# Kernel optimization log

Hardware: AMD Instinct MI355X
Metric: run time of the kernel (lower is better)

The kernel has to match this reference:

```python
import jax, jax.numpy as jnp
import numpy as np

EMBED_DIM = 512
BLOCK = 511
N_HEAD = 8
N_GLOBAL = 4
N_LOCAL = 2
N_MIX = 2
RECEP = 4
T = 2 * BLOCK + 2  # [task, clip, BLOCK upper, BLOCK lower]
HD = EMBED_DIM // N_HEAD
NEG = -1e9


def _build_masks():
    bs = BLOCK
    temporal = np.concatenate([np.zeros(2), np.arange(bs) * 2 + 1, np.arange(bs) * 2 + 2])
    seq = temporal[None, :] <= temporal[:, None]  # causal over interleaved temporal order
    tq = np.concatenate([np.arange(bs) * 2 + 1 - 2 * RECEP + 1] * 2)
    tk = np.concatenate([np.arange(bs) * 2 + 1] * 2)
    de = tk[None, :] < tq[:, None]  # keys too far in the past for the sliding window
    local = seq.copy()
    local[2:, 2:] = local[2:, 2:] & ~de
    return jnp.asarray(local), jnp.asarray(seq)


LOCAL_MASK, GLOBAL_MASK = _build_masks()  # (T, T) bool, True = visible


def _linear_params(key, fan_in, fan_out):
    k1, k2 = jax.random.split(key)
    s = 1.0 / np.sqrt(fan_in)
    W = jax.random.uniform(k1, (fan_out, fan_in), minval=-s, maxval=s, dtype=jnp.float32)
    b = jax.random.uniform(k2, (fan_out,), minval=-s, maxval=s, dtype=jnp.float32)
    return W, b


def setup_inputs() -> dict:
    key = jax.random.key(0)
    ks = jax.random.split(key, 10)
    B = 4
    x = jax.random.normal(ks[0], (B, T, EMBED_DIM), dtype=jnp.float32)
    cond_mask = jnp.ones((B, T), dtype=jnp.float32)
    Wq, bq = _linear_params(ks[1], EMBED_DIM, EMBED_DIM)
    Wk, bk = _linear_params(ks[2], EMBED_DIM, EMBED_DIM)
    Wv, bv = _linear_params(ks[3], EMBED_DIM, EMBED_DIM)
    Wqml, bqml = _linear_params(ks[4], EMBED_DIM, HD * N_MIX)
    Wkml, bkml = _linear_params(ks[5], EMBED_DIM, HD * N_MIX)
    Wp, bp = _linear_params(ks[6], EMBED_DIM, EMBED_DIM)
    mix_w = jax.random.normal(ks[7], (N_MIX, 2), dtype=jnp.float32) * 0.5  # Conv2d(2*nm, nm, groups=nm, 1x1)
    bias_clip = jnp.full((1, N_HEAD, 1), 0.5, dtype=jnp.float32)
    bias_clip_ml = jnp.full((1, N_MIX, 1), 0.5, dtype=jnp.float32)
    return dict(x=x, cond_mask=cond_mask, Wq=Wq, bq=bq, Wk=Wk, bk=bk, Wv=Wv, bv=bv,
                Wqml=Wqml, bqml=bqml, Wkml=Wkml, bkml=bkml, mix_w=mix_w, Wp=Wp, bp=bp,
                bias_clip=bias_clip, bias_clip_ml=bias_clip_ml)


def reference(x, cond_mask, Wq, bq, Wk, bk, Wv, bv, Wqml, bqml, Wkml, bkml, mix_w, Wp, bp, bias_clip, bias_clip_ml):
    B, Tx, C = x.shape

    def heads(W, b, nh):
        return (x @ W.T + b).reshape(B, Tx, nh, HD).transpose(0, 2, 1, 3)  # (B, nh, T, hd)

    q = heads(Wq, bq, N_HEAD)
    k = heads(Wk, bk, N_HEAD)
    v = heads(Wv, bv, N_HEAD)
    qml = heads(Wqml, bqml, N_MIX)
    kml = heads(Wkml, bkml, N_MIX)

    scale = 1.0 / np.sqrt(HD)
    # main attention: heads [0:N_LOCAL] local-masked, rest global (causal) masked
    att = jnp.einsum('bhqd,bhkd->bhqk', q, k) * scale
    att = att.at[:, :, :, 1].add(bias_clip)  # learned bias on the CLIP-token key column
    head_mask = jnp.concatenate([
        jnp.broadcast_to(LOCAL_MASK, (N_LOCAL, Tx, Tx)),
        jnp.broadcast_to(GLOBAL_MASK, (N_MIX + N_GLOBAL, Tx, Tx))], axis=0)
    att = jax.nn.softmax(jnp.where(head_mask[None], att, NEG), axis=-1)

    # extra local-masked score maps for the mix heads
    aml = jnp.einsum('bhqd,bhkd->bhqk', qml, kml) * scale
    aml = aml.at[:, :, :, 1].add(bias_clip_ml)
    aml = jax.nn.softmax(jnp.where(LOCAL_MASK[None, None], aml, NEG), axis=-1)

    # grouped 1x1 conv: per mix head, blend (global, local) attention maps
    mix_in = jnp.stack([att[:, N_LOCAL:N_LOCAL + N_MIX], aml], axis=2)  # (B, nm, 2, T, T)
    mix_out = jnp.einsum('ho,bhoqk->bhqk', mix_w, mix_in)

    att_f = jnp.concatenate([att[:, :N_LOCAL], mix_out, att[:, N_LOCAL + N_MIX:]], axis=1)
    y = jnp.einsum('bhqk,bhkd->bhqd', att_f, v)
    y = y.transpose(0, 2, 1, 3).reshape(B, Tx, C)
    return y @ Wp.T + bp
```

## Files before the change

kernel.cpp:

```cpp
#include <hip/hip_runtime.h>

typedef unsigned short u16;
typedef __attribute__((ext_vector_type(8))) __bf16 bf16x8;
typedef __attribute__((ext_vector_type(4))) float f32x4;
typedef __attribute__((ext_vector_type(8))) short short8;
typedef __attribute__((ext_vector_type(4))) u16 us4;

#define T_SEQ 1024
#define PW 1280

__device__ __forceinline__ u16 f2bf(float f) {
  unsigned u = __float_as_uint(f);
  u += 0x7fff + ((u >> 16) & 1);
  return (u16)(u >> 16);
}
__device__ __forceinline__ float bf2f(u16 v) {
  return __uint_as_float((unsigned)v << 16);
}

__constant__ u16 GLOB_M[16] = {0x0101,0x0303,0x0707,0x0F0F,0x1F1F,0x3F3F,0x7F7F,0xFFFF,
                               0xFFFF,0x0307,0x070F,0x0F1F,0x1F3F,0x3F7F,0x7FFF,0xFFFF};
__constant__ u16 LOC_M[16]  = {0x0101,0x0303,0x0607,0x0C0D,0x1819,0x3031,0x6061,0xC0C1,
                               0x8183,0x0307,0x060F,0x0C1D,0x1839,0x3071,0x60E1,0xC1C1};

__device__ __forceinline__ void gll16(const u16* gp, u16* lp) {
  __builtin_amdgcn_global_load_lds((const __attribute__((address_space(1))) unsigned*)gp,
                                   (__attribute__((address_space(3))) unsigned*)lp, 16, 0, 0);
}

template<int NISS>
__device__ __forceinline__ void stage_sw(u16* lds, const u16* __restrict__ g,
                                         int ld, int tid) {
  const int w = tid >> 6;
#pragma unroll
  for (int i = 0; i < NISS; ++i) {
    int row = i * 32 + (tid >> 3);
    int cswz = ((tid & 7) << 4) ^ ((row & 7) << 4);
    gll16(g + (size_t)row * ld + (cswz >> 1), lds + i * 2048 + w * 512);
  }
}

__device__ __forceinline__ void stage8(u16* lds, const u16* __restrict__ g,
                                       int ld, int tid) {
  int row = tid >> 3;
  int cswz = (((tid & 7) << 4) ^ ((row & 7) << 4)) >> 1;
  gll16(g + (size_t)row * ld + cswz, lds + (tid >> 6) * 512);
}

__device__ __forceinline__ bf16x8 rd_sw(const u16* lds, int row, int colbyte) {
  return *(const bf16x8*)&lds[row * 64 + ((colbyte ^ ((row & 7) << 4)) >> 1)];
}

__global__ void prep_all(const float4* __restrict__ x, u16* __restrict__ xb,
                         const float* __restrict__ Wq, const float* __restrict__ Wk,
                         const float* __restrict__ Wv, const float* __restrict__ Wqml,
                         const float* __restrict__ Wkml, const float* __restrict__ Wp,
                         const float* __restrict__ bq, const float* __restrict__ bk,
                         const float* __restrict__ bv, const float* __restrict__ bqml,
                         const float* __restrict__ bkml,
                         u16* __restrict__ Wcat, u16* __restrict__ Wpx, float* __restrict__ bcat) {
  if (blockIdx.x < 2048) {
    int i = blockIdx.x * 256 + threadIdx.x;
    float4 v = x[i];
    us4 o = { f2bf(v.x), f2bf(v.y), f2bf(v.z), f2bf(v.w) };
    *(us4*)&xb[i * 4] = o;
    return;
  }
  int idx = (blockIdx.x - 2048) * 256 + threadIdx.x;
  const int NW = 1792 * 512;
  if (idx < NW) {
    int row = idx >> 9;
    float v;
    if (row < 512)       v = Wq[idx];
    else if (row < 1024) v = Wk[idx - 512 * 512];
    else if (row < 1536) v = Wv[idx - 1024 * 512];
    else if (row < 1664) v = Wqml[idx - 1536 * 512];
    else                 v = Wkml[idx - 1664 * 512];
    Wcat[idx] = f2bf(v);
    return;
  }
  int i2 = idx - NW;
  if (i2 < 512 * 640) {
    int n = i2 / 640, k2 = i2 - n * 640;
    float v = (k2 < 512) ? Wp[n * 512 + k2] : Wp[n * 512 + k2 - 384];
    Wpx[i2] = f2bf(v);
    return;
  }
  int i3 = i2 - 512 * 640;
  if (i3 < 1792) {
    float v;
    if (i3 < 512)       v = bq[i3];
    else if (i3 < 1024) v = bk[i3 - 512];
    else if (i3 < 1536) v = bv[i3 - 1024];
    else if (i3 < 1664) v = bqml[i3 - 1536];
    else                v = bkml[i3 - 1664];
    bcat[i3] = v;
  }
}

__global__ __launch_bounds__(256) void gemm_qkv(
    const u16* __restrict__ A, const u16* __restrict__ Bw,
    const float* __restrict__ bias, u16* __restrict__ Pout, u16* __restrict__ Vtb) {
  __shared__ u16 As[2][8192];
  __shared__ u16 Bs[2][8192];
  const int tid = threadIdx.x;
  const int lane = tid & 63, w = tid >> 6;
  const int g = lane >> 4, c = lane & 15;
  const int n0 = blockIdx.x * 128, m0 = blockIdx.y * 128;
  const int wm = (w >> 1) * 64, wn = (w & 1) * 64;

  f32x4 acc[4][4] = {};
  stage_sw<4>(As[0], A + (size_t)m0 * 512, 512, tid);
  stage_sw<4>(Bs[0], Bw + (size_t)n0 * 512, 512, tid);
  __syncthreads();
  for (int ks = 0; ks < 8; ++ks) {
    int cur = ks & 1;
    if (ks + 1 < 8) {
      stage_sw<4>(As[cur ^ 1], A + (size_t)m0 * 512 + (ks + 1) * 64, 512, tid);
      stage_sw<4>(Bs[cur ^ 1], Bw + (size_t)n0 * 512 + (ks + 1) * 64, 512, tid);
    }
#pragma unroll
    for (int h = 0; h < 2; ++h) {
      bf16x8 av[4], bv[4];
#pragma unroll
      for (int f = 0; f < 4; ++f) {
        av[f] = rd_sw(As[cur], wm + f * 16 + c, h * 64 + g * 16);
        bv[f] = rd_sw(Bs[cur], wn + f * 16 + c, h * 64 + g * 16);
      }
#pragma unroll
      for (int fm = 0; fm < 4; ++fm)
#pragma unroll
        for (int fn = 0; fn < 4; ++fn)
          acc[fm][fn] = __builtin_amdgcn_mfma_f32_16x16x32_bf16(av[fm], bv[fn], acc[fm][fn], 0, 0, 0);
    }
    __syncthreads();
  }

  const bool isV = (n0 >= 1024 && n0 < 1536);
#pragma unroll
  for (int fm = 0; fm < 4; ++fm)
#pragma unroll
    for (int fn = 0; fn < 4; ++fn) {
      int row = m0 + wm + fm * 16 + g * 4;
      int col = n0 + wn + fn * 16 + c;
      float bb = bias[col];
      if (isV) {
        int d = col - 1024;
        int bidx = row >> 10, t = row & 1023;
        us4 pack = { f2bf(acc[fm][fn][0] + bb), f2bf(acc[fm][fn][1] + bb),
                     f2bf(acc[fm][fn][2] + bb), f2bf(acc[fm][fn][3] + bb) };
        *(us4*)&Vtb[((size_t)bidx * 512 + d) * 1024 + t] = pack;
      } else {
        int pcol = (col < 1024) ? col : col - 512;
#pragma unroll
        for (int r = 0; r < 4; ++r)
          Pout[(size_t)(row + r) * PW + pcol] = f2bf(acc[fm][fn][r] + bb);
      }
    }
}

__global__ __launch_bounds__(256) void gemm_out(
    const u16* __restrict__ A, const u16* __restrict__ Bw,
    const float* __restrict__ bias, float* __restrict__ Cout) {
  __shared__ u16 As[2][8192];
  __shared__ u16 Bs[2][4096];
  const int tid = threadIdx.x;
  const int lane = tid & 63, w = tid >> 6;
  const int g = lane >> 4, c = lane & 15;
  const int n0 = blockIdx.x * 64, m0 = blockIdx.y * 128;
  const int wm = (w >> 1) * 64, wn = (w & 1) * 32;

  f32x4 acc[4][2] = {};
  stage_sw<4>(As[0], A + (size_t)m0 * 640, 640, tid);
  stage_sw<2>(Bs[0], Bw + (size_t)n0 * 640, 640, tid);
  __syncthreads();
  for (int ks = 0; ks < 10; ++ks) {
    int cur = ks & 1;
    if (ks + 1 < 10) {
      stage_sw<4>(As[cur ^ 1], A + (size_t)m0 * 640 + (ks + 1) * 64, 640, tid);
      stage_sw<2>(Bs[cur ^ 1], Bw + (size_t)n0 * 640 + (ks + 1) * 64, 640, tid);
    }
#pragma unroll
    for (int h = 0; h < 2; ++h) {
      bf16x8 av[4], bv[2];
#pragma unroll
      for (int f = 0; f < 4; ++f)
        av[f] = rd_sw(As[cur], wm + f * 16 + c, h * 64 + g * 16);
#pragma unroll
      for (int f = 0; f < 2; ++f)
        bv[f] = rd_sw(Bs[cur], wn + f * 16 + c, h * 64 + g * 16);
#pragma unroll
      for (int fm = 0; fm < 4; ++fm)
#pragma unroll
        for (int fn = 0; fn < 2; ++fn)
          acc[fm][fn] = __builtin_amdgcn_mfma_f32_16x16x32_bf16(av[fm], bv[fn], acc[fm][fn], 0, 0, 0);
    }
    __syncthreads();
  }
#pragma unroll
  for (int fm = 0; fm < 4; ++fm)
#pragma unroll
    for (int fn = 0; fn < 2; ++fn)
#pragma unroll
      for (int r = 0; r < 4; ++r) {
        int row = m0 + wm + fm * 16 + g * 4 + r;
        int col = n0 + wn + fn * 16 + c;
        Cout[(size_t)row * 512 + col] = acc[fm][fn][r] + bias[col];
      }
}

__global__ __launch_bounds__(512, 6) void attn_k(
    const u16* __restrict__ P, const u16* __restrict__ Vtb, u16* __restrict__ Y,
    u16* __restrict__ Part_o, float* __restrict__ Part_ml,
    const float* __restrict__ mix_w, const float* __restrict__ bias_clip,
    const float* __restrict__ bias_clip_ml) {
  __shared__ u16 Ks[2][4096];
  __shared__ u16 Vs[2][4096];
  __shared__ u16 Ps[8][1152];
  const int tid = threadIdx.x, lane = tid & 63, w = tid >> 6;
  const int g = lane >> 4, c = lane & 15;
  const int qt2 = blockIdx.x, u = blockIdx.y, b = blockIdx.z;

  int qcol, kcol, vsel, outcol = 0, slot = -1;
  bool localMask = false;
  float kbias, wgt = 1.0f;
  unsigned mask;
  if (u < 24) {
    int h = 2 + (u >> 2), sp = u & 3; slot = u;
    qcol = h * 64; kcol = 512 + h * 64; vsel = h; kbias = bias_clip[h];
    mask = ((unsigned)GLOB_M[2 * qt2] | (unsigned)GLOB_M[2 * qt2 + 1]) & (0x1111u << sp);
  } else if (u < 26) {
    int h = u - 24;
    qcol = h * 64; kcol = 512 + h * 64; vsel = h; outcol = h * 64;
    localMask = true; kbias = bias_clip[h];
    mask = (unsigned)LOC_M[2 * qt2] | (unsigned)LOC_M[2 * qt2 + 1];
  } else {
    int mh = u - 26;
    qcol = 1024 + mh * 64; kcol = 1152 + mh * 64; vsel = 2 + mh; outcol = 512 + mh * 64;
    localMask = true; kbias = bias_clip_ml[mh]; wgt = mix_w[mh * 2 + 1];
    mask = (unsigned)LOC_M[2 * qt2] | (unsigned)LOC_M[2 * qt2 + 1];
  }
  const size_t baseP = (size_t)b * T_SEQ * PW;
  const u16* __restrict__ Kbase = P + baseP + kcol;
  const u16* __restrict__ Vbase = Vtb + ((size_t)b * 512 + vsel * 64) * 1024;
  const int r0 = qt2 * 128 + w * 16;
  const int qg = r0 + c;

  int tq = (qg < 2) ? 0 : ((qg < 513) ? 2 * qg - 3 : 2 * qg - 1024);
  int upmax = (tq - 1) >> 1;
  int lomax = (tq - 2) >> 1;
  int wmin = (localMask && qg >= 2) ? ((qg < 513 ? qg - 2 : qg - 513) - 3) : -1000000;

  float mM = -1e8f, lL = 0.0f;
  f32x4 o[4] = {};

  if (mask) {
    bf16x8 aq0 = *(const bf16x8*)&P[baseP + (size_t)qg * PW + qcol + g * 8];
    bf16x8 aq1 = *(const bf16x8*)&P[baseP + (size_t)qg * PW + qcol + 32 + g * 8];

    unsigned rem = mask;
    int kt_cur = __ffs(rem) - 1; rem &= rem - 1;
    stage8(Ks[0], Kbase + (size_t)(kt_cur * 64) * PW, PW, tid);
    stage8(Vs[0], Vbase + kt_cur * 64, 1024, tid);
    int kt_nxt = -1;
    if (rem) {
      kt_nxt = __ffs(rem) - 1; rem &= rem - 1;
      stage8(Ks[1], Kbase + (size_t)(kt_nxt * 64) * PW, PW, tid);
      stage8(Vs[1], Vbase + kt_nxt * 64, 1024, tid);
    }
    int cur = 0;

    for (;;) {
      if (kt_nxt >= 0) asm volatile("s_waitcnt vmcnt(2)" ::: "memory");
      else             asm volatile("s_waitcnt vmcnt(0)" ::: "memory");
      __builtin_amdgcn_sched_barrier(0);
      __builtin_amdgcn_s_barrier();

      const int k0 = kt_cur * 64;

      float s[4][4];
#pragma unroll
      for (int cb = 0; cb < 4; ++cb) {
        f32x4 accs = {};
        bf16x8 bk0 = rd_sw(Ks[cur], cb * 16 + c, g * 16);
        bf16x8 bk1 = rd_sw(Ks[cur], cb * 16 + c, 64 + g * 16);
        accs = __builtin_amdgcn_mfma_f32_16x16x32_bf16(bk0, aq0, accs, 0, 0, 0);
        accs = __builtin_amdgcn_mfma_f32_16x16x32_bf16(bk1, aq1, accs, 0, 0, 0);
#pragma unroll
        for (int r = 0; r < 4; ++r) s[cb][r] = accs[r] * 0.125f;
      }

#pragma unroll
      for (int cb = 0; cb < 4; ++cb) {
        int kb = k0 + cb * 16 + g * 4;
#pragma unroll
        for (int r = 0; r < 4; ++r) {
          int kk = kb + r;
          bool tok = kk < 2;
          bool low = kk >= 513;
          int jk = kk - (low ? 513 : 2);
          int bnd = low ? lomax : upmax;
          bool vis = tok | ((jk <= bnd) & (jk >= wmin));
          float addb = (kk == 1) ? kbias : 0.0f;
          s[cb][r] = vis ? (s[cb][r] + addb) : -1e9f;
        }
      }

      float rmax = s[0][0];
#pragma unroll
      for (int cb = 0; cb < 4; ++cb)
#pragma unroll
        for (int r = 0; r < 4; ++r) rmax = fmaxf(rmax, s[cb][r]);
      rmax = fmaxf(rmax, __shfl_xor(rmax, 16));
      rmax = fmaxf(rmax, __shfl_xor(rmax, 32));
      float mnew = fmaxf(mM, rmax);
      float fr = __expf(mM - mnew);
      float psum = 0.0f;
#pragma unroll
      for (int cb = 0; cb < 4; ++cb)
#pragma unroll
        for (int r = 0; r < 4; ++r) {
          float p = __expf(s[cb][r] - mnew);
          s[cb][r] = p;
          psum += p;
        }
      psum += __shfl_xor(psum, 16);
      psum += __shfl_xor(psum, 32);
      lL = lL * fr + psum;
      mM = mnew;
#pragma unroll
      for (int db = 0; db < 4; ++db) o[db] *= fr;

#pragma unroll
      for (int cb = 0; cb < 4; ++cb) {
        us4 pk = { f2bf(s[cb][0]), f2bf(s[cb][1]), f2bf(s[cb][2]), f2bf(s[cb][3]) };
        *(us4*)&Ps[w][c * 72 + cb * 16 + g * 4] = pk;
      }
      asm volatile("s_waitcnt lgkmcnt(0)" ::: "memory");
      __builtin_amdgcn_sched_barrier(0);

#pragma unroll
      for (int ks2 = 0; ks2 < 2; ++ks2) {
        bf16x8 ap = *(const bf16x8*)&Ps[w][c * 72 + ks2 * 32 + g * 8];
#pragma unroll
        for (int db = 0; db < 4; ++db) {
          bf16x8 av = rd_sw(Vs[cur], db * 16 + c, ks2 * 64 + g * 16);
          o[db] = __builtin_amdgcn_mfma_f32_16x16x32_bf16(av, ap, o[db], 0, 0, 0);
        }
      }

      __builtin_amdgcn_s_barrier();
      if (kt_nxt < 0) break;
      int kt_nn = -1;
      if (rem) {
        kt_nn = __ffs(rem) - 1; rem &= rem - 1;
        stage8(Ks[cur], Kbase + (size_t)(kt_nn * 64) * PW, PW, tid);
        stage8(Vs[cur], Vbase + kt_nn * 64, 1024, tid);
      }
      kt_cur = kt_nxt; kt_nxt = kt_nn; cur ^= 1;
    }
  }

  if (slot >= 0) {
    u16* po = Part_o + ((size_t)(slot * 4 + b)) * T_SEQ * 64;
#pragma unroll
    for (int db = 0; db < 4; ++db) {
      us4 pk = { f2bf(o[db][0]), f2bf(o[db][1]), f2bf(o[db][2]), f2bf(o[db][3]) };
      *(us4*)&po[(size_t)qg * 64 + db * 16 + g * 4] = pk;
    }
    if (g == 0) {
      float2 ml = { mM, lL };
      *(float2*)&Part_ml[(((size_t)(slot * 4 + b)) * T_SEQ + qg) * 2] = ml;
    }
  } else {
    float wl = wgt / lL;
#pragma unroll
    for (int db = 0; db < 4; ++db) {
      us4 pk = { f2bf(o[db][0] * wl), f2bf(o[db][1] * wl),
                 f2bf(o[db][2] * wl), f2bf(o[db][3] * wl) };
      *(us4*)&Y[((size_t)b * T_SEQ + qg) * 640 + outcol + db * 16 + g * 4] = pk;
    }
  }
}

__global__ __launch_bounds__(256) void combine_k(
    const u16* __restrict__ Part_o, const float* __restrict__ Part_ml,
    u16* __restrict__ Y, const float* __restrict__ mix_w) {
  int idx = blockIdx.x * 256 + threadIdx.x;
  int q4 = idx & 15;
  int row = (idx >> 4) & 1023;
  int bb = (idx >> 14) & 3;
  int hp = idx >> 16;
  float mv[4], lv[4];
  float ms = -1e30f;
#pragma unroll
  for (int s = 0; s < 4; ++s) {
    size_t base = (((size_t)(hp * 4 + s) * 4 + bb) * 1024 + row) * 2;
    mv[s] = Part_ml[base];
    lv[s] = Part_ml[base + 1];
    ms = fmaxf(ms, mv[s]);
  }
  float denom = 0.0f, e[4];
#pragma unroll
  for (int s = 0; s < 4; ++s) { e[s] = __expf(mv[s] - ms); denom += lv[s] * e[s]; }
  float wgt = (hp < 2) ? mix_w[hp * 2] : 1.0f;
  float inv = wgt / denom;
  float out[4] = {0.f, 0.f, 0.f, 0.f};
#pragma unroll
  for (int s = 0; s < 4; ++s) {
    us4 ov = *(const us4*)&Part_o[(((size_t)(hp * 4 + s) * 4 + bb) * 1024 + row) * 64 + q4 * 4];
#pragma unroll
    for (int j = 0; j < 4; ++j) out[j] += e[s] * bf2f(ov[j]);
  }
  us4 pk = { f2bf(out[0] * inv), f2bf(out[1] * inv), f2bf(out[2] * inv), f2bf(out[3] * inv) };
  *(us4*)&Y[((size_t)bb * 1024 + row) * 640 + (hp + 2) * 64 + q4 * 4] = pk;
}

extern "C" void kernel_launch(void* const* d_in, const int* in_sizes, int n_in,
                              void* d_out, int out_size, void* d_ws, size_t ws_size,
                              hipStream_t stream) {
  const float* x     = (const float*)d_in[0];
  const float* Wq    = (const float*)d_in[2];
  const float* bq    = (const float*)d_in[3];
  const float* Wk    = (const float*)d_in[4];
  const float* bk    = (const float*)d_in[5];
  const float* Wv    = (const float*)d_in[6];
  const float* bv    = (const float*)d_in[7];
  const float* Wqml  = (const float*)d_in[8];
  const float* bqml  = (const float*)d_in[9];
  const float* Wkml  = (const float*)d_in[10];
  const float* bkml  = (const float*)d_in[11];
  const float* mixw  = (const float*)d_in[12];
  const float* Wp    = (const float*)d_in[13];
  const float* bp    = (const float*)d_in[14];
  const float* bclip = (const float*)d_in[15];
  const float* bclipml = (const float*)d_in[16];

  u16* xb   = (u16*)d_ws;
  u16* Wcat = xb + 4096 * 512;
  u16* Wpx  = Wcat + 1792 * 512;
  u16* Ybuf = Wpx + 512 * 640;
  u16* Vtb  = Ybuf + 4096 * 640;
  u16* Pbuf = Vtb + 4 * 512 * 1024;
  float* bcat = (float*)(Pbuf + 4096 * 1280);
  u16* Part_o = (u16*)(bcat + 2048);
  float* Part_ml = (float*)(Part_o + 24 * 4 * 1024 * 64);

  prep_all<<<6919, 256, 0, stream>>>((const float4*)x, xb, Wq, Wk, Wv, Wqml, Wkml, Wp,
                                     bq, bk, bv, bqml, bkml, Wcat, Wpx, bcat);
  gemm_qkv<<<dim3(14, 32), 256, 0, stream>>>(xb, Wcat, bcat, Pbuf, Vtb);
  attn_k<<<dim3(8, 28, 4), 512, 0, stream>>>(Pbuf, Vtb, Ybuf, Part_o, Part_ml,
                                             mixw, bclip, bclipml);
  combine_k<<<1536, 256, 0, stream>>>(Part_o, Part_ml, Ybuf, mixw);
  gemm_out<<<dim3(8, 32), 256, 0, stream>>>(Ybuf, Wpx, bp, (float*)d_out);
}
```

Before: 80.65 us.

## Split local heads across key chunks, fold scale into Q, keep P in registers

Local-masked and mix heads are now split into two key-tile partitions each, so all 32 work units write partial (o, m, l) results and combine_k merges a variable number of splits. The softmax scale and log2(e) are folded into Q during the QKV GEMM epilogue so attention can use exp2 without a per-score multiply. The P matrix is converted with packed bf16 conversion and redistributed via lane shuffles instead of a round trip through LDS. Occupancy hint raised to 8 blocks. The cost is more partial-output traffic and a larger combine pass.

```diff
diff --git a/kernel.cpp b/kernel.cpp
--- a/kernel.cpp
+++ b/kernel.cpp
@@ -5,9 +5,12 @@
 typedef __attribute__((ext_vector_type(4))) float f32x4;
 typedef __attribute__((ext_vector_type(8))) short short8;
 typedef __attribute__((ext_vector_type(4))) u16 us4;
+typedef __attribute__((ext_vector_type(4))) unsigned u32x4;
 
 #define T_SEQ 1024
 #define PW 1280
+#define QSC 0.18033688f
+#define L2E 1.4426950408889634f
 
 __device__ __forceinline__ u16 f2bf(float f) {
   unsigned u = __float_as_uint(f);
@@ -151,10 +154,11 @@
                      f2bf(acc[fm][fn][2] + bb), f2bf(acc[fm][fn][3] + bb) };
         *(us4*)&Vtb[((size_t)bidx * 512 + d) * 1024 + t] = pack;
       } else {
+        float sc = (col < 512 || (col >= 1536 && col < 1664)) ? QSC : 1.0f;
         int pcol = (col < 1024) ? col : col - 512;
 #pragma unroll
         for (int r = 0; r < 4; ++r)
-          Pout[(size_t)(row + r) * PW + pcol] = f2bf(acc[fm][fn][r] + bb);
+          Pout[(size_t)(row + r) * PW + pcol] = f2bf((acc[fm][fn][r] + bb) * sc);
       }
     }
 }
@@ -209,37 +213,38 @@
       }
 }
 
-__global__ __launch_bounds__(512, 6) void attn_k(
-    const u16* __restrict__ P, const u16* __restrict__ Vtb, u16* __restrict__ Y,
+__global__ __launch_bounds__(512, 8) void attn_k(
+    const u16* __restrict__ P, const u16* __restrict__ Vtb,
     u16* __restrict__ Part_o, float* __restrict__ Part_ml,
-    const float* __restrict__ mix_w, const float* __restrict__ bias_clip,
-    const float* __restrict__ bias_clip_ml) {
+    const float* __restrict__ bias_clip, const float* __restrict__ bias_clip_ml) {
   __shared__ u16 Ks[2][4096];
   __shared__ u16 Vs[2][4096];
-  __shared__ u16 Ps[8][1152];
   const int tid = threadIdx.x, lane = tid & 63, w = tid >> 6;
   const int g = lane >> 4, c = lane & 15;
   const int qt2 = blockIdx.x, u = blockIdx.y, b = blockIdx.z;
 
-  int qcol, kcol, vsel, outcol = 0, slot = -1;
-  bool localMask = false;
-  float kbias, wgt = 1.0f;
+  int qcol, kcol, vsel;
+  bool localMask;
+  float kbias;
   unsigned mask;
+  unsigned uni = (unsigned)LOC_M[2 * qt2] | (unsigned)LOC_M[2 * qt2 + 1];
   if (u < 24) {
-    int h = 2 + (u >> 2), sp = u & 3; slot = u;
+    int h = 2 + (u >> 2), sp = u & 3;
     qcol = h * 64; kcol = 512 + h * 64; vsel = h; kbias = bias_clip[h];
+    localMask = false;
     mask = ((unsigned)GLOB_M[2 * qt2] | (unsigned)GLOB_M[2 * qt2 + 1]) & (0x1111u << sp);
-  } else if (u < 26) {
-    int h = u - 24;
-    qcol = h * 64; kcol = 512 + h * 64; vsel = h; outcol = h * 64;
-    localMask = true; kbias = bias_clip[h];
-    mask = (unsigned)LOC_M[2 * qt2] | (unsigned)LOC_M[2 * qt2 + 1];
+  } else if (u < 28) {
+    int h = (u - 24) >> 1, sp = (u - 24) & 1;
+    qcol = h * 64; kcol = 512 + h * 64; vsel = h; kbias = bias_clip[h];
+    localMask = true;
+    mask = uni & (sp ? 0xAAAAu : 0x5555u);
   } else {
-    int mh = u - 26;
-    qcol = 1024 + mh * 64; kcol = 1152 + mh * 64; vsel = 2 + mh; outcol = 512 + mh * 64;
-    localMask = true; kbias = bias_clip_ml[mh]; wgt = mix_w[mh * 2 + 1];
-    mask = (unsigned)LOC_M[2 * qt2] | (unsigned)LOC_M[2 * qt2 + 1];
-  }
+    int mh = (u - 28) >> 1, sp = (u - 28) & 1;
+    qcol = 1024 + mh * 64; kcol = 1152 + mh * 64; vsel = 2 + mh; kbias = bias_clip_ml[mh];
+    localMask = true;
+    mask = uni & (sp ? 0xAAAAu : 0x5555u);
+  }
+  kbias *= L2E;
   const size_t baseP = (size_t)b * T_SEQ * PW;
   const u16* __restrict__ Kbase = P + baseP + kcol;
   const u16* __restrict__ Vbase = Vtb + ((size_t)b * 512 + vsel * 64) * 1024;
@@ -287,7 +292,7 @@
         accs = __builtin_amdgcn_mfma_f32_16x16x32_bf16(bk0, aq0, accs, 0, 0, 0);
         accs = __builtin_amdgcn_mfma_f32_16x16x32_bf16(bk1, aq1, accs, 0, 0, 0);
 #pragma unroll
-        for (int r = 0; r < 4; ++r) s[cb][r] = accs[r] * 0.125f;
+        for (int r = 0; r < 4; ++r) s[cb][r] = accs[r];
       }
 
 #pragma unroll
@@ -314,13 +319,13 @@
       rmax = fmaxf(rmax, __shfl_xor(rmax, 16));
       rmax = fmaxf(rmax, __shfl_xor(rmax, 32));
       float mnew = fmaxf(mM, rmax);
-      float fr = __expf(mM - mnew);
+      float fr = exp2f(mM - mnew);
       float psum = 0.0f;
 #pragma unroll
       for (int cb = 0; cb < 4; ++cb)
 #pragma unroll
         for (int r = 0; r < 4; ++r) {
-          float p = __expf(s[cb][r] - mnew);
+          float p = exp2f(s[cb][r] - mnew);
           s[cb][r] = p;
           psum += p;
         }
@@ -331,17 +336,29 @@
 #pragma unroll
       for (int db = 0; db < 4; ++db) o[db] *= fr;
 
+      unsigned wpk[4][2];
 #pragma unroll
       for (int cb = 0; cb < 4; ++cb) {
-        us4 pk = { f2bf(s[cb][0]), f2bf(s[cb][1]), f2bf(s[cb][2]), f2bf(s[cb][3]) };
-        *(us4*)&Ps[w][c * 72 + cb * 16 + g * 4] = pk;
-      }
-      asm volatile("s_waitcnt lgkmcnt(0)" ::: "memory");
-      __builtin_amdgcn_sched_barrier(0);
-
+        asm("v_cvt_pk_bf16_f32 %0, %1, %2" : "=v"(wpk[cb][0]) : "v"(s[cb][0]), "v"(s[cb][1]));
+        asm("v_cvt_pk_bf16_f32 %0, %1, %2" : "=v"(wpk[cb][1]) : "v"(s[cb][2]), "v"(s[cb][3]));
+      }
 #pragma unroll
       for (int ks2 = 0; ks2 < 2; ++ks2) {
-        bf16x8 ap = *(const bf16x8*)&Ps[w][c * 72 + ks2 * 32 + g * 8];
+        unsigned tw[4];
+#pragma unroll
+        for (int rr = 0; rr < 2; ++rr) {
+          unsigned L = wpk[2 * ks2][rr], H = wpk[2 * ks2 + 1][rr];
+          unsigned sA = (g & 1) ? L : H;
+          unsigned sB = (g & 1) ? H : L;
+          unsigned X16 = (unsigned)__shfl_xor((int)sA, 16);
+          unsigned X32 = (unsigned)__shfl_xor((int)sA, 32);
+          unsigned X48 = (unsigned)__shfl_xor((int)sB, 48);
+          unsigned a  = (g >= 2) ? ((g == 3) ? X16 : X32) : ((g == 1) ? X48 : L);
+          unsigned b2 = (g >= 2) ? ((g == 3) ? H : X48) : ((g == 1) ? X32 : X16);
+          tw[rr] = a; tw[2 + rr] = b2;
+        }
+        u32x4 tw4 = { tw[0], tw[1], tw[2], tw[3] };
+        bf16x8 ap = __builtin_bit_cast(bf16x8, tw4);
 #pragma unroll
         for (int db = 0; db < 4; ++db) {
           bf16x8 av = rd_sw(Vs[cur], db * 16 + c, ks2 * 64 + g * 16);
@@ -361,25 +378,15 @@
     }
   }
 
-  if (slot >= 0) {
-    u16* po = Part_o + ((size_t)(slot * 4 + b)) * T_SEQ * 64;
-#pragma unroll
-    for (int db = 0; db < 4; ++db) {
-      us4 pk = { f2bf(o[db][0]), f2bf(o[db][1]), f2bf(o[db][2]), f2bf(o[db][3]) };
-      *(us4*)&po[(size_t)qg * 64 + db * 16 + g * 4] = pk;
-    }
-    if (g == 0) {
-      float2 ml = { mM, lL };
-      *(float2*)&Part_ml[(((size_t)(slot * 4 + b)) * T_SEQ + qg) * 2] = ml;
-    }
-  } else {
-    float wl = wgt / lL;
-#pragma unroll
-    for (int db = 0; db < 4; ++db) {
-      us4 pk = { f2bf(o[db][0] * wl), f2bf(o[db][1] * wl),
-                 f2bf(o[db][2] * wl), f2bf(o[db][3] * wl) };
-      *(us4*)&Y[((size_t)b * T_SEQ + qg) * 640 + outcol + db * 16 + g * 4] = pk;
-    }
+  u16* po = Part_o + ((size_t)(u * 4 + b)) * T_SEQ * 64;
+#pragma unroll
+  for (int db = 0; db < 4; ++db) {
+    us4 pk = { f2bf(o[db][0]), f2bf(o[db][1]), f2bf(o[db][2]), f2bf(o[db][3]) };
+    *(us4*)&po[(size_t)qg * 64 + db * 16 + g * 4] = pk;
+  }
+  if (g == 0) {
+    float2 ml = { mM, lL };
+    *(float2*)&Part_ml[(((size_t)(u * 4 + b)) * T_SEQ + qg) * 2] = ml;
   }
 }
 
@@ -390,30 +397,32 @@
   int q4 = idx & 15;
   int row = (idx >> 4) & 1023;
   int bb = (idx >> 14) & 3;
-  int hp = idx >> 16;
+  int j = idx >> 16;
+  int ns, bs, outcol;
+  float wgt;
+  if (j < 6)      { ns = 4; bs = j * 4;            outcol = 128 + j * 64;       wgt = (j < 2) ? mix_w[2 * j] : 1.0f; }
+  else if (j < 8) { ns = 2; bs = 24 + (j - 6) * 2; outcol = (j - 6) * 64;       wgt = 1.0f; }
+  else            { ns = 2; bs = 28 + (j - 8) * 2; outcol = 512 + (j - 8) * 64; wgt = mix_w[(j - 8) * 2 + 1]; }
+
   float mv[4], lv[4];
   float ms = -1e30f;
-#pragma unroll
-  for (int s = 0; s < 4; ++s) {
-    size_t base = (((size_t)(hp * 4 + s) * 4 + bb) * 1024 + row) * 2;
+  for (int s = 0; s < ns; ++s) {
+    size_t base = (((size_t)(bs + s) * 4 + bb) * 1024 + row) * 2;
     mv[s] = Part_ml[base];
     lv[s] = Part_ml[base + 1];
     ms = fmaxf(ms, mv[s]);
   }
   float denom = 0.0f, e[4];
-#pragma unroll
-  for (int s = 0; s < 4; ++s) { e[s] = __expf(mv[s] - ms); denom += lv[s] * e[s]; }
-  float wgt = (hp < 2) ? mix_w[hp * 2] : 1.0f;
+  for (int s = 0; s < ns; ++s) { e[s] = exp2f(mv[s] - ms); denom += lv[s] * e[s]; }
   float inv = wgt / denom;
   float out[4] = {0.f, 0.f, 0.f, 0.f};
-#pragma unroll
-  for (int s = 0; s < 4; ++s) {
-    us4 ov = *(const us4*)&Part_o[(((size_t)(hp * 4 + s) * 4 + bb) * 1024 + row) * 64 + q4 * 4];
-#pragma unroll
-    for (int j = 0; j < 4; ++j) out[j] += e[s] * bf2f(ov[j]);
+  for (int s = 0; s < ns; ++s) {
+    us4 ov = *(const us4*)&Part_o[(((size_t)(bs + s) * 4 + bb) * 1024 + row) * 64 + q4 * 4];
+#pragma unroll
+    for (int t = 0; t < 4; ++t) out[t] += e[s] * bf2f(ov[t]);
   }
   us4 pk = { f2bf(out[0] * inv), f2bf(out[1] * inv), f2bf(out[2] * inv), f2bf(out[3] * inv) };
-  *(us4*)&Y[((size_t)bb * 1024 + row) * 640 + (hp + 2) * 64 + q4 * 4] = pk;
+  *(us4*)&Y[((size_t)bb * 1024 + row) * 640 + outcol + q4 * 4] = pk;
 }
 
 extern "C" void kernel_launch(void* const* d_in, const int* in_sizes, int n_in,
@@ -444,13 +453,12 @@
   u16* Pbuf = Vtb + 4 * 512 * 1024;
   float* bcat = (float*)(Pbuf + 4096 * 1280);
   u16* Part_o = (u16*)(bcat + 2048);
-  float* Part_ml = (float*)(Part_o + 24 * 4 * 1024 * 64);
+  float* Part_ml = (float*)(Part_o + 32 * 4 * 1024 * 64);
 
   prep_all<<<6919, 256, 0, stream>>>((const float4*)x, xb, Wq, Wk, Wv, Wqml, Wkml, Wp,
                                      bq, bk, bv, bqml, bkml, Wcat, Wpx, bcat);
   gemm_qkv<<<dim3(14, 32), 256, 0, stream>>>(xb, Wcat, bcat, Pbuf, Vtb);
-  attn_k<<<dim3(8, 28, 4), 512, 0, stream>>>(Pbuf, Vtb, Ybuf, Part_o, Part_ml,
-                                             mixw, bclip, bclipml);
-  combine_k<<<1536, 256, 0, stream>>>(Part_o, Part_ml, Ybuf, mixw);
+  attn_k<<<dim3(8, 32, 4), 512, 0, stream>>>(Pbuf, Vtb, Part_o, Part_ml, bclip, bclipml);
+  combine_k<<<2560, 256, 0, stream>>>(Part_o, Part_ml, Ybuf, mixw);
   gemm_out<<<dim3(8, 32), 256, 0, stream>>>(Ybuf, Wpx, bp, (float*)d_out);
 }
```

Result: slower. 83.97 us (+4.1%).
